# Kernel optimization log

Measured on AMD Instinct MI355X. Metric: run time of the kernel, lower is better.

The kernel has to match this reference:

```python
import jax, jax.numpy as jnp
import numpy as np

EMBED = 1024
HEADS = 16


def setup_inputs() -> dict:
    key = jax.random.key(0)
    ks = jax.random.split(key, 12)
    N, S, E = 8, 1024, EMBED
    s = 1.0 / np.sqrt(E)
    inp = {
        'queries': jax.random.normal(ks[0], (N, S, E), jnp.float32),
        'keys': jax.random.normal(ks[1], (N, S, E), jnp.float32),
        'values': jax.random.normal(ks[2], (N, S, E), jnp.float32),
        'Wq': jax.random.normal(ks[3], (E, E), jnp.float32) * s,
        'bq': jax.random.normal(ks[4], (E,), jnp.float32) * s,
        'Wk': jax.random.normal(ks[5], (E, E), jnp.float32) * s,
        'bk': jax.random.normal(ks[6], (E,), jnp.float32) * s,
        'Wv': jax.random.normal(ks[7], (E, E), jnp.float32) * s,
        'bv': jax.random.normal(ks[8], (E,), jnp.float32) * s,
        'Wo': jax.random.normal(ks[9], (E, E), jnp.float32) * s,
        'bo': jax.random.normal(ks[10], (E,), jnp.float32) * s,
    }
    return inp


def reference(queries, keys, values, Wq, bq, Wk, bk, Wv, bv, Wo, bo):
    N, S, E = queries.shape
    H = HEADS
    D = E // H
    # linear projections (torch Linear: x @ W.T + b)
    q = queries @ Wq.T + bq
    k = keys @ Wk.T + bk
    v = values @ Wv.T + bv
    q = q.reshape(N, S, H, D)
    k = k.reshape(N, S, H, D)
    v = v.reshape(N, S, H, D)
    # NOTE: original scales by sqrt(embed_size), not sqrt(head_dim)
    scores = jnp.einsum('nqhd,nkhd->nhqk', q, k) / jnp.sqrt(jnp.float32(E))
    attn = jax.nn.softmax(scores, axis=3)
    out = jnp.einsum('nhqk,nkhd->nqhd', attn, v).reshape(N, S, E)
    return out @ Wo.T + bo
```

## Files before the change

### kernel.cpp

```cpp
#include <hip/hip_runtime.h>


typedef unsigned short ushort_t;
typedef __bf16 bf16_8 __attribute__((ext_vector_type(8)));
typedef float f32x4 __attribute__((ext_vector_type(4)));
typedef unsigned short ushort8 __attribute__((ext_vector_type(8)));
typedef short short8v __attribute__((ext_vector_type(8)));

#define SEQ  1024
#define EMB  1024
#define NBAT 8
#define NH   16
#define HD   64
#define MROW (NBAT * SEQ)

__device__ __forceinline__ ushort_t cvt_bf16(float x) {
  unsigned u = __float_as_uint(x);
  u += 0x7FFFu + ((u >> 16) & 1u);
  return (ushort_t)(u >> 16);
}
__device__ __forceinline__ float bf2f(ushort_t u) {
  return __uint_as_float(((unsigned)u) << 16);
}
__device__ __forceinline__ short f2bs(float x) {
  return __builtin_bit_cast(short, (__bf16)x);
}

__device__ __forceinline__ void async_copy16(const ushort_t* g, ushort_t* l) {
  __builtin_amdgcn_global_load_lds(
      (const __attribute__((address_space(1))) void*)g,
      (__attribute__((address_space(3))) void*)l, 16, 0, 0);
}

__global__ void dtype_probe(const ushort_t* __restrict__ w, int* __restrict__ flag) {
  __shared__ int cnt;
  if (threadIdx.x == 0) cnt = 0;
  __syncthreads();
  int c = 0;
  for (int i = threadIdx.x; i < 4096; i += 256) {
    const int e = (w[i] >> 7) & 0xFF;
    if (e >= 129) ++c;
  }
  atomicAdd(&cnt, c);
  __syncthreads();
  if (threadIdx.x == 0) *flag = (cnt > 256) ? 1 : 0;
}

__device__ __forceinline__ ushort8 load8(const void* base, size_t off, bool f32) {
  if (f32) {
    const float* p = (const float*)base + off;
    const f32x4 a = *(const f32x4*)p;
    const f32x4 b = *(const f32x4*)(p + 4);
    ushort8 r;
    r[0] = cvt_bf16(a[0]); r[1] = cvt_bf16(a[1]);
    r[2] = cvt_bf16(a[2]); r[3] = cvt_bf16(a[3]);
    r[4] = cvt_bf16(b[0]); r[5] = cvt_bf16(b[1]);
    r[6] = cvt_bf16(b[2]); r[7] = cvt_bf16(b[3]);
    return r;
  }
  return *(const ushort8*)((const ushort_t*)base + off);
}

__global__ __launch_bounds__(256)
void convert_all(const void* __restrict__ q, const void* __restrict__ k,
                 const void* __restrict__ v, const void* __restrict__ wq,
                 const void* __restrict__ wk, const void* __restrict__ wv,
                 const void* __restrict__ wo,
                 ushort_t* __restrict__ cq, ushort_t* __restrict__ ck,
                 ushort_t* __restrict__ cv, ushort_t* __restrict__ cwq,
                 ushort_t* __restrict__ cwk, ushort_t* __restrict__ cwv,
                 ushort_t* __restrict__ cwo, const int* __restrict__ flag) {
  const bool f32 = (*flag != 0);
  const int b = blockIdx.x;
  const void* src;
  ushort_t* dst;
  int boff;
  if (b < 12288) {
    const int t = b >> 12;
    boff = b & 4095;
    src = (t == 0) ? q : (t == 1) ? k : v;
    dst = (t == 0) ? cq : (t == 1) ? ck : cv;
  } else {
    const int t = (b - 12288) >> 9;
    boff = (b - 12288) & 511;
    src = (t == 0) ? wq : (t == 1) ? wk : (t == 2) ? wv : wo;
    dst = (t == 0) ? cwq : (t == 1) ? cwk : (t == 2) ? cwv : cwo;
  }
  const size_t i = (size_t)boff * 256 + threadIdx.x;
  *(ushort8*)(dst + i * 8) = load8(src, i * 8, f32);
}

__device__ __forceinline__ void gemm_body(
    ushort_t* As, ushort_t* Bs,
    const ushort_t* __restrict__ A, const ushort_t* __restrict__ B,
    const void* __restrict__ bias, void* __restrict__ Cout, bool f32,
    int bm, int bn, int mode) {
  const int tid  = threadIdx.x;
  const int lane = tid & 63;
  const int wave = tid >> 6;
  const int wm = wave & 1, wn = wave >> 1;
  const int col  = lane & 15;
  const int quad = lane >> 4;

  const ushort_t* Ab = A + (size_t)bm * EMB;
  const ushort_t* Bb = B + (size_t)bn * EMB;

  float bvv[4];
  if (mode != 1) {
#pragma unroll
    for (int nt = 0; nt < 4; ++nt) {
      const int i = bn + wn * 64 + nt * 16 + col;
      bvv[nt] = f32 ? ((const float*)bias)[i] : bf2f(((const ushort_t*)bias)[i]);
    }
  }

  f32x4 acc[4][4] = {};

  for (int kb = 0; kb < EMB; kb += 32) {
#pragma unroll
    for (int j = 0; j < 2; ++j) {
      const int s   = j * 256 + tid;
      const int row = s >> 2;
      const int ch  = (s & 3) << 3;
      const int s0  = j * 256 + wave * 64;
      async_copy16(Ab + (size_t)row * EMB + kb + ch, &As[s0 * 8]);
      async_copy16(Bb + (size_t)row * EMB + kb + ch, &Bs[s0 * 8]);
    }
    __syncthreads();

    bf16_8 af[4], bfr[4];
#pragma unroll
    for (int mt = 0; mt < 4; ++mt)
      af[mt] = *(const bf16_8*)(As + (wm * 64 + mt * 16 + col) * 32 + quad * 8);
#pragma unroll
    for (int nt = 0; nt < 4; ++nt)
      bfr[nt] = *(const bf16_8*)(Bs + (wn * 64 + nt * 16 + col) * 32 + quad * 8);
#pragma unroll
    for (int mt = 0; mt < 4; ++mt)
#pragma unroll
      for (int nt = 0; nt < 4; ++nt)
        acc[mt][nt] = __builtin_amdgcn_mfma_f32_16x16x32_bf16(af[mt], bfr[nt],
                                                              acc[mt][nt], 0, 0, 0);
    __syncthreads();
  }

#pragma unroll
  for (int mt = 0; mt < 4; ++mt)
#pragma unroll
    for (int nt = 0; nt < 4; ++nt) {
      const int gcol = bn + wn * 64 + nt * 16 + col;
#pragma unroll
      for (int r = 0; r < 4; ++r) {
        const int grow = bm + wm * 64 + mt * 16 + quad * 4 + r;
        if (mode == 1) {
          const float bb =
              f32 ? ((const float*)bias)[grow] : bf2f(((const ushort_t*)bias)[grow]);
          const float vv = acc[mt][nt][r] + bb;
          const int nn = gcol >> 10, ss = gcol & 1023;
          const int hh = grow >> 6,  dd = grow & 63;
          ((ushort_t*)Cout)[(size_t)((nn * NH + hh) * HD + dd) * SEQ + ss] =
              cvt_bf16(vv);
        } else {
          const float vv = acc[mt][nt][r] + bvv[nt];
          const size_t idx = (size_t)grow * EMB + gcol;
          if (mode == 2 && f32) ((float*)Cout)[idx] = vv;
          else                  ((ushort_t*)Cout)[idx] = cvt_bf16(vv);
        }
      }
    }
}

__global__ __launch_bounds__(256)
void gemm_qkv(const ushort_t* __restrict__ cq, const ushort_t* __restrict__ ck,
              const ushort_t* __restrict__ cv, const ushort_t* __restrict__ cWq,
              const ushort_t* __restrict__ cWk, const ushort_t* __restrict__ cWv,
              const void* __restrict__ bq, const void* __restrict__ bk,
              const void* __restrict__ bv, void* __restrict__ Qp,
              void* __restrict__ Kp, void* __restrict__ Vt,
              const int* __restrict__ flag) {
  __shared__ __align__(16) ushort_t As[128 * 32];
  __shared__ __align__(16) ushort_t Bs[128 * 32];
  const bool f32 = (*flag != 0);
  const int t = blockIdx.x >> 9;
  const int bid = blockIdx.x & 511;
  if (t == 0)
    gemm_body(As, Bs, cq, cWq, bq, Qp, f32, (bid & 63) << 7, (bid >> 6) << 7, 0);
  else if (t == 1)
    gemm_body(As, Bs, ck, cWk, bk, Kp, f32, (bid & 63) << 7, (bid >> 6) << 7, 0);
  else
    gemm_body(As, Bs, cWv, cv, bv, Vt, f32, (bid & 7) << 7, (bid >> 3) << 7, 1);
}

__global__ __launch_bounds__(256)
void gemm_one(const ushort_t* __restrict__ A, const ushort_t* __restrict__ B,
              const void* __restrict__ bias, void* __restrict__ Cout,
              const int* __restrict__ flag, int mode) {
  __shared__ __align__(16) ushort_t As[128 * 32];
  __shared__ __align__(16) ushort_t Bs[128 * 32];
  gemm_body(As, Bs, A, B, bias, Cout, (*flag != 0),
            (blockIdx.x & 63) << 7, (blockIdx.x >> 6) << 7, mode);
}

template <int MODE>
__global__ __launch_bounds__(256)
void gemm_flex(const void* __restrict__ A, const void* __restrict__ B,
               const void* __restrict__ bias, void* __restrict__ Cout,
               const int* __restrict__ flag, int a_ext, int final_out) {
  __shared__ __align__(16) ushort_t As[128 * 32];
  __shared__ __align__(16) ushort_t Bs[128 * 32];
  const bool f32  = (*flag != 0);
  const bool af32 = f32 && (a_ext != 0);
  const int tid  = threadIdx.x;
  const int lane = tid & 63;
  const int wave = tid >> 6;
  const int wm = wave & 1, wn = wave >> 1;
  const int col  = lane & 15;
  const int quad = lane >> 4;
  const int bm = (blockIdx.x & 63) << 7;
  const int bn = (blockIdx.x >> 6) << 7;

  f32x4 acc[4][4] = {};

  for (int kb = 0; kb < EMB; kb += 32) {
    ushort8 ra[2], rb[2];
#pragma unroll
    for (int j = 0; j < 2; ++j) {
      const int s   = j * 256 + tid;
      const int row = s >> 2;
      const int ch  = (s & 3) << 3;
      ra[j] = load8(A, (size_t)(bm + row) * EMB + kb + ch, af32);
      rb[j] = load8(B, (size_t)(bn + row) * EMB + kb + ch, f32);
    }
#pragma unroll
    for (int j = 0; j < 2; ++j) {
      const int s = j * 256 + tid;
      *(ushort8*)(As + s * 8) = ra[j];
      *(ushort8*)(Bs + s * 8) = rb[j];
    }
    __syncthreads();

    bf16_8 af[4], bfr[4];
#pragma unroll
    for (int mt = 0; mt < 4; ++mt)
      af[mt] = *(const bf16_8*)(As + (wm * 64 + mt * 16 + col) * 32 + quad * 8);
#pragma unroll
    for (int nt = 0; nt < 4; ++nt)
      bfr[nt] = *(const bf16_8*)(Bs + (wn * 64 + nt * 16 + col) * 32 + quad * 8);
#pragma unroll
    for (int mt = 0; mt < 4; ++mt)
#pragma unroll
      for (int nt = 0; nt < 4; ++nt)
        acc[mt][nt] = __builtin_amdgcn_mfma_f32_16x16x32_bf16(af[mt], bfr[nt],
                                                              acc[mt][nt], 0, 0, 0);
    __syncthreads();
  }

  float bvv[4];
#pragma unroll
  for (int nt = 0; nt < 4; ++nt) {
    const int i = bn + wn * 64 + nt * 16 + col;
    bvv[nt] = f32 ? ((const float*)bias)[i] : bf2f(((const ushort_t*)bias)[i]);
  }
#pragma unroll
  for (int mt = 0; mt < 4; ++mt)
#pragma unroll
    for (int nt = 0; nt < 4; ++nt) {
      const int gcol = bn + wn * 64 + nt * 16 + col;
#pragma unroll
      for (int r = 0; r < 4; ++r) {
        const int grow = bm + wm * 64 + mt * 16 + quad * 4 + r;
        const float vv = acc[mt][nt][r] + bvv[nt];
        if (MODE == 0) {
          const size_t idx = (size_t)grow * EMB + gcol;
          if (final_out && f32) ((float*)Cout)[idx] = vv;
          else                  ((ushort_t*)Cout)[idx] = cvt_bf16(vv);
        } else {
          const int nn = grow >> 10, ss = grow & 1023;
          const int hh = gcol >> 6,  dd = gcol & 63;
          ((ushort_t*)Cout)[(size_t)((nn * NH + hh) * HD + dd) * SEQ + ss] =
              cvt_bf16(vv);
        }
      }
    }
}

__global__ __launch_bounds__(256)
void attn_kernel(const ushort_t* __restrict__ Q, const ushort_t* __restrict__ K,
                 const ushort_t* __restrict__ V, ushort_t* __restrict__ O) {
  const int tid  = threadIdx.x;
  const int lane = tid & 63;
  const int wave = tid >> 6;
  const int col  = lane & 15;
  const int quad = lane >> 4;
  const int gid = blockIdx.x;
  const int nh  = gid & 127;
  const int qb  = gid >> 7;
  const int h  = nh & 15;
  const int n  = nh >> 4;
  const int q0 = qb * 256 + wave * 64;

  bf16_8 aq0[4], aq1[4];
#pragma unroll
  for (int g = 0; g < 4; ++g) {
    const ushort_t* qp =
        Q + (size_t)(n * SEQ + q0 + g * 16 + col) * EMB + h * HD + quad * 8;
    aq0[g] = *(const bf16_8*)qp;
    aq1[g] = *(const bf16_8*)(qp + 32);
  }

  const int sig = ((col >> 2) << 3) | (col & 3);
  const ushort_t* kp = K + (size_t)(n * SEQ + sig) * EMB + h * HD + quad * 8;
  const ushort_t* vp = V + ((size_t)nh * HD + col) * SEQ + quad * 8;

  f32x4 acc[4][4] = {};
  float lsum[4] = {0.f, 0.f, 0.f, 0.f};

  const float SCL = 0.04508422f;
  const float MOF = 16.0f;

#define ATTN_LOAD(KX, VX, KB_)                                               \
  do {                                                                       \
    const ushort_t* kpi = kp + (size_t)(KB_) * EMB;                          \
    KX[0] = *(const bf16_8*)(kpi);                                           \
    KX[1] = *(const bf16_8*)(kpi + 32);                                      \
    KX[2] = *(const bf16_8*)(kpi + 4 * EMB);                                 \
    KX[3] = *(const bf16_8*)(kpi + 4 * EMB + 32);                            \
    _Pragma("unroll")                                                        \
    for (int dt = 0; dt < 4; ++dt)                                           \
      VX[dt] = *(const bf16_8*)(vp + (size_t)dt * 16 * SEQ + (KB_));         \
  } while (0)

#define ATTN_TILE(KX, VX)                                                    \
  do {                                                                       \
    _Pragma("unroll")                                                        \
    for (int g = 0; g < 4; ++g) {                                            \
      const f32x4 z = {};                                                    \
      __builtin_amdgcn_s_setprio(1);                                         \
      f32x4 s0 = __builtin_amdgcn_mfma_f32_16x16x32_bf16(KX[0], aq0[g], z, 0, 0, 0); \
      s0 = __builtin_amdgcn_mfma_f32_16x16x32_bf16(KX[1], aq1[g], s0, 0, 0, 0);      \
      f32x4 s1 = __builtin_amdgcn_mfma_f32_16x16x32_bf16(KX[2], aq0[g], z, 0, 0, 0); \
      s1 = __builtin_amdgcn_mfma_f32_16x16x32_bf16(KX[3], aq1[g], s1, 0, 0, 0);      \
      __builtin_amdgcn_s_setprio(0);                                         \
      short8v pas;                                                           \
      _Pragma("unroll")                                                      \
      for (int r = 0; r < 4; ++r) {                                          \
        const float p0 = __builtin_amdgcn_exp2f(__builtin_fmaf(s0[r], SCL, -MOF)); \
        const float p1 = __builtin_amdgcn_exp2f(__builtin_fmaf(s1[r], SCL, -MOF)); \
        lsum[g] += p0 + p1;                                                  \
        pas[r]     = f2bs(p0);                                               \
        pas[r + 4] = f2bs(p1);                                               \
      }                                                                      \
      const bf16_8 pab = __builtin_bit_cast(bf16_8, pas);                    \
      __builtin_amdgcn_s_setprio(1);                                         \
      _Pragma("unroll")                                                      \
      for (int dt = 0; dt < 4; ++dt)                                         \
        acc[g][dt] = __builtin_amdgcn_mfma_f32_16x16x32_bf16(pab, VX[dt], acc[g][dt], 0, 0, 0); \
      __builtin_amdgcn_s_setprio(0);                                         \
    }                                                                        \
  } while (0)

  bf16_8 KA[4], KB2[4], VA[4], VB[4];

  ATTN_LOAD(KA, VA, 0);
  for (int kb = 0; kb < SEQ; kb += 64) {
    ATTN_LOAD(KB2, VB, kb + 32);
    __builtin_amdgcn_sched_barrier(0);
    ATTN_TILE(KA, VA);
    if (kb + 64 < SEQ) {
      ATTN_LOAD(KA, VA, kb + 64);
      __builtin_amdgcn_sched_barrier(0);
    }
    ATTN_TILE(KB2, VB);
  }

#undef ATTN_LOAD
#undef ATTN_TILE

#pragma unroll
  for (int g = 0; g < 4; ++g) {
    float tot = lsum[g];
    tot += __shfl_xor(tot, 16, 64);
    tot += __shfl_xor(tot, 32, 64);
    float rinv[4];
#pragma unroll
    for (int r = 0; r < 4; ++r)
      rinv[r] = 1.0f / __shfl(tot, quad * 4 + r, 16);
#pragma unroll
    for (int dt = 0; dt < 4; ++dt)
#pragma unroll
      for (int r = 0; r < 4; ++r)
        O[(size_t)(n * SEQ + q0 + g * 16 + quad * 4 + r) * EMB + h * HD +
          dt * 16 + col] = cvt_bf16(acc[g][dt][r] * rinv[r]);
  }
}

extern "C" void kernel_launch(void* const* d_in, const int* in_sizes, int n_in,
                              void* d_out, int out_size, void* d_ws, size_t ws_size,
                              hipStream_t stream) {
  const void* q  = d_in[0];
  const void* k  = d_in[1];
  const void* v  = d_in[2];
  const void* Wq = d_in[3];
  const void* bq = d_in[4];
  const void* Wk = d_in[5];
  const void* bk = d_in[6];
  const void* Wv = d_in[7];
  const void* bv = d_in[8];
  const void* Wo = d_in[9];
  const void* bo = d_in[10];

  const size_t TE = (size_t)MROW * EMB;
  const size_t WE = (size_t)EMB * EMB;
  int* flag = (int*)d_ws;
  char* base = (char*)d_ws + 256;
  const size_t NEED = 256 + (4 * TE + 4 * WE) * sizeof(ushort_t);

  const dim3 tB(256);
  dtype_probe<<<dim3(1), tB, 0, stream>>>((const ushort_t*)Wq, flag);

  if (ws_size >= NEED) {
    ushort_t* cq  = (ushort_t*)base;
    ushort_t* ck  = cq + TE;
    ushort_t* cv  = ck + TE;
    ushort_t* Qp  = cv + TE;
    ushort_t* cWq = Qp + TE;
    ushort_t* cWk = cWq + WE;
    ushort_t* cWv = cWk + WE;
    ushort_t* cWo = cWv + WE;
    ushort_t* Kp  = (ushort_t*)d_out;
    ushort_t* Vt  = (ushort_t*)d_out + TE;
    ushort_t* Oa  = Qp;

    convert_all<<<dim3(14336), tB, 0, stream>>>(q, k, v, Wq, Wk, Wv, Wo,
                                                cq, ck, cv, cWq, cWk, cWv, cWo,
                                                flag);
    gemm_qkv<<<dim3(1536), tB, 0, stream>>>(cq, ck, cv, cWq, cWk, cWv,
                                            bq, bk, bv, Qp, Kp, Vt, flag);
    attn_kernel<<<dim3(512), tB, 0, stream>>>(Qp, Kp, Vt, Oa);
    gemm_one<<<dim3(512), tB, 0, stream>>>(Oa, cWo, bo, d_out, flag, 2);
  } else {
    ushort_t* Qp = (ushort_t*)base;
    ushort_t* Vt = Qp + TE;
    ushort_t* Kp = (ushort_t*)d_out;
    ushort_t* Oa = Qp;
    const dim3 gB(512);
    gemm_flex<0><<<gB, tB, 0, stream>>>(q, Wq, bq, Qp, flag, 1, 0);
    gemm_flex<0><<<gB, tB, 0, stream>>>(k, Wk, bk, Kp, flag, 1, 0);
    gemm_flex<1><<<gB, tB, 0, stream>>>(v, Wv, bv, Vt, flag, 1, 0);
    attn_kernel<<<dim3(512), tB, 0, stream>>>(Qp, Kp, Vt, Oa);
    gemm_flex<0><<<gB, tB, 0, stream>>>(Oa, Wo, bo, d_out, flag, 0, 1);
  }
}
```

Baseline: 332.4 us.

## Double-buffer LDS tiles in projection GEMMs to overlap loads with MFMA

```diff
diff --git a/kernel.cpp b/kernel.cpp
--- a/kernel.cpp
+++ b/kernel.cpp
@@ -91,7 +91,7 @@
 }
 
 __device__ __forceinline__ void gemm_body(
-    ushort_t* As, ushort_t* Bs,
+    ushort_t* As0, ushort_t* Bs0, ushort_t* As1, ushort_t* Bs1,
     const ushort_t* __restrict__ A, const ushort_t* __restrict__ B,
     const void* __restrict__ bias, void* __restrict__ Cout, bool f32,
     int bm, int bn, int mode) {
@@ -116,33 +116,55 @@
 
   f32x4 acc[4][4] = {};
 
-  for (int kb = 0; kb < EMB; kb += 32) {
-#pragma unroll
-    for (int j = 0; j < 2; ++j) {
-      const int s   = j * 256 + tid;
-      const int row = s >> 2;
-      const int ch  = (s & 3) << 3;
-      const int s0  = j * 256 + wave * 64;
-      async_copy16(Ab + (size_t)row * EMB + kb + ch, &As[s0 * 8]);
-      async_copy16(Bb + (size_t)row * EMB + kb + ch, &Bs[s0 * 8]);
-    }
+#define GEMM_STAGE(Asx, Bsx, KB_)                                            \
+  do {                                                                       \
+    _Pragma("unroll")                                                        \
+    for (int j = 0; j < 2; ++j) {                                            \
+      const int s   = j * 256 + tid;       \
+      const int row = s >> 2;                                                \
+      const int ch  = (s & 3) << 3;                                          \
+      const int s0  = j * 256 + wave * 64;   \
+      async_copy16(Ab + (size_t)row * EMB + (KB_) + ch, &Asx[s0 * 8]);       \
+      async_copy16(Bb + (size_t)row * EMB + (KB_) + ch, &Bsx[s0 * 8]);       \
+    }                                                                        \
+  } while (0)
+
+#define GEMM_COMPUTE(Asx, Bsx)                                               \
+  do {                                                                       \
+    bf16_8 af[4], bfr[4];                                                    \
+    _Pragma("unroll")                                                        \
+    for (int mt = 0; mt < 4; ++mt)                                           \
+      af[mt] = *(const bf16_8*)(Asx + (wm * 64 + mt * 16 + col) * 32 + quad * 8); \
+    _Pragma("unroll")                                                        \
+    for (int nt = 0; nt < 4; ++nt)                                           \
+      bfr[nt] = *(const bf16_8*)(Bsx + (wn * 64 + nt * 16 + col) * 32 + quad * 8); \
+    _Pragma("unroll")                                                        \
+    for (int mt = 0; mt < 4; ++mt)                                           \
+      _Pragma("unroll")                                                      \
+      for (int nt = 0; nt < 4; ++nt)                                         \
+        acc[mt][nt] = __builtin_amdgcn_mfma_f32_16x16x32_bf16(af[mt], bfr[nt], \
+                                                              acc[mt][nt], 0, 0, 0); \
+  } while (0)
+
+  GEMM_STAGE(As0, Bs0, 0);
+  __syncthreads();
+
+  for (int kb = 0; kb < EMB; kb += 64) {
+    GEMM_STAGE(As1, Bs1, kb + 32);
+    __builtin_amdgcn_sched_barrier(0);
+    GEMM_COMPUTE(As0, Bs0);
     __syncthreads();
 
-    bf16_8 af[4], bfr[4];
-#pragma unroll
-    for (int mt = 0; mt < 4; ++mt)
-      af[mt] = *(const bf16_8*)(As + (wm * 64 + mt * 16 + col) * 32 + quad * 8);
-#pragma unroll
-    for (int nt = 0; nt < 4; ++nt)
-      bfr[nt] = *(const bf16_8*)(Bs + (wn * 64 + nt * 16 + col) * 32 + quad * 8);
-#pragma unroll
-    for (int mt = 0; mt < 4; ++mt)
-#pragma unroll
-      for (int nt = 0; nt < 4; ++nt)
-        acc[mt][nt] = __builtin_amdgcn_mfma_f32_16x16x32_bf16(af[mt], bfr[nt],
-                                                              acc[mt][nt], 0, 0, 0);
+    if (kb + 64 < EMB) {
+      GEMM_STAGE(As0, Bs0, kb + 64);
+      __builtin_amdgcn_sched_barrier(0);
+    }
+    GEMM_COMPUTE(As1, Bs1);
     __syncthreads();
   }
+
+#undef GEMM_STAGE
+#undef GEMM_COMPUTE
 
 #pragma unroll
   for (int mt = 0; mt < 4; ++mt)
@@ -178,26 +200,33 @@
               const void* __restrict__ bv, void* __restrict__ Qp,
               void* __restrict__ Kp, void* __restrict__ Vt,
               const int* __restrict__ flag) {
-  __shared__ __align__(16) ushort_t As[128 * 32];
-  __shared__ __align__(16) ushort_t Bs[128 * 32];
+  __shared__ __align__(16) ushort_t As0[128 * 32];
+  __shared__ __align__(16) ushort_t Bs0[128 * 32];
+  __shared__ __align__(16) ushort_t As1[128 * 32];
+  __shared__ __align__(16) ushort_t Bs1[128 * 32];
   const bool f32 = (*flag != 0);
   const int t = blockIdx.x >> 9;
   const int bid = blockIdx.x & 511;
   if (t == 0)
-    gemm_body(As, Bs, cq, cWq, bq, Qp, f32, (bid & 63) << 7, (bid >> 6) << 7, 0);
+    gemm_body(As0, Bs0, As1, Bs1, cq, cWq, bq, Qp, f32,
+              (bid & 63) << 7, (bid >> 6) << 7, 0);
   else if (t == 1)
-    gemm_body(As, Bs, ck, cWk, bk, Kp, f32, (bid & 63) << 7, (bid >> 6) << 7, 0);
+    gemm_body(As0, Bs0, As1, Bs1, ck, cWk, bk, Kp, f32,
+              (bid & 63) << 7, (bid >> 6) << 7, 0);
   else
-    gemm_body(As, Bs, cWv, cv, bv, Vt, f32, (bid & 7) << 7, (bid >> 3) << 7, 1);
+    gemm_body(As0, Bs0, As1, Bs1, cWv, cv, bv, Vt, f32,
+              (bid & 7) << 7, (bid >> 3) << 7, 1);
 }
 
 __global__ __launch_bounds__(256)
 void gemm_one(const ushort_t* __restrict__ A, const ushort_t* __restrict__ B,
               const void* __restrict__ bias, void* __restrict__ Cout,
               const int* __restrict__ flag, int mode) {
-  __shared__ __align__(16) ushort_t As[128 * 32];
-  __shared__ __align__(16) ushort_t Bs[128 * 32];
-  gemm_body(As, Bs, A, B, bias, Cout, (*flag != 0),
+  __shared__ __align__(16) ushort_t As0[128 * 32];
+  __shared__ __align__(16) ushort_t Bs0[128 * 32];
+  __shared__ __align__(16) ushort_t As1[128 * 32];
+  __shared__ __align__(16) ushort_t Bs1[128 * 32];
+  gemm_body(As0, Bs0, As1, Bs1, A, B, bias, Cout, (*flag != 0),
             (blockIdx.x & 63) << 7, (blockIdx.x >> 6) << 7, mode);
 }
 
```

Measured after the change: 333.0 us. Within noise of the previous version (+0.2%).
